# Optimization experiments

Hardware: AMD Instinct MI355X
Metric: run time of the kernel (lower is better)

Reference implementation:

```python
import jax, jax.numpy as jnp
import numpy as np

H = 16  # num_heads


def _sinusoidal_positions(n_pos, d, dtype=jnp.float32):
    half = d // 2
    freqs = 1.0 / 10000 ** (jnp.arange(0, half, dtype=dtype) / float(half))
    pos = jnp.arange(n_pos, dtype=dtype)[:, None]
    angles = pos * freqs[None, :]
    emb = jnp.concatenate([jnp.sin(angles), jnp.cos(angles)], axis=-1)
    if d % 2 == 1:
        emb = jnp.pad(emb, ((0, 0), (0, 1)))
    return emb.astype(dtype)


def setup_inputs() -> dict:
    key = jax.random.key(0)
    B, M, C = 64, 2048, 1024
    D = C // H
    ks = jax.random.split(key, 12)
    s = 1.0 / np.sqrt(C)
    return {
        "x": jax.random.normal(ks[0], (B, C), jnp.float32),
        "mem": jax.random.normal(ks[1], (B, M, C), jnp.float32),
        "Wq": jax.random.normal(ks[2], (C, C), jnp.float32) * s,
        "bq": jnp.zeros((C,), jnp.float32),
        "Wk": jax.random.normal(ks[3], (C, C), jnp.float32) * s,
        "bk": jnp.zeros((C,), jnp.float32),
        "Wv": jax.random.normal(ks[4], (C, C), jnp.float32) * s,
        "bv": jnp.zeros((C,), jnp.float32),
        "u_bias": jax.random.normal(ks[5], (H, D), jnp.float32) * 0.02,
        "v_bias": jax.random.normal(ks[6], (H, D), jnp.float32) * 0.02,
        "Wo": jax.random.normal(ks[7], (C, C), jnp.float32) * s,
        "bo": jnp.zeros((C,), jnp.float32),
    }


def reference(x, mem, Wq, bq, Wk, bk, Wv, bv, u_bias, v_bias, Wo, bo):
    B, C = x.shape
    D = C // H
    M = mem.shape[1]
    L = M + 1
    cat = jnp.concatenate([mem, x[:, None, :]], axis=1)  # (B, L, C)
    q = (x @ Wq + bq).reshape(B, H, D)
    k = (cat @ Wk + bk).reshape(B, L, H, D)
    v = (cat @ Wv + bv).reshape(B, L, H, D)
    r = _sinusoidal_positions(L, D)[::-1, :]  # (L, D), reversed
    scale = 1.0 / jnp.sqrt(jnp.float32(D))
    ac = jnp.einsum('bhd,blhd->bhl', q + u_bias[None, :, :], k)
    bd = jnp.einsum('bhd,ld->bhl', q + v_bias[None, :, :], r)
    attn = jax.nn.softmax((ac + bd) * scale, axis=-1)
    out = jnp.einsum('bhl,blhd->bhd', attn, v).reshape(B, C)
    return out @ Wo + bo
```

## Files before the change

kernel.cpp:

```cpp
#include <hip/hip_runtime.h>
#include <hip/hip_bf16.h>
#include <math.h>

#define B   64
#define C   1024
#define HH  16
#define DD  64
#define MM  2048
#define LL  2049
#define SCALE 0.125f
#define NCHC 9
#define CHC  228

template <int CTRL>
__device__ __forceinline__ float dpp_add(float keep, float send) {
  int moved =
      __builtin_amdgcn_update_dpp(0, __float_as_int(send), CTRL, 0xF, 0xF, true);
  return keep + __int_as_float(moved);
}

__global__ __launch_bounds__(256) void k_gemm(
    const float* __restrict__ A, int a_row_stride, int a_bx_off,
    const float* __restrict__ W, float* __restrict__ P) {
  __shared__ __attribute__((aligned(16))) float a_s[64 * 132];
  __shared__ __attribute__((aligned(16))) float b_s[128 * 68];
  int t = threadIdx.x;
  int jt = blockIdx.x, kc = blockIdx.y;
  const float* Ab = A + (size_t)jt * a_bx_off;
  int k0 = kc * 128;
  for (int idx = t; idx < 2048; idx += 256) {
    int bb = idx >> 5, f4 = idx & 31;
    float4 v = *(const float4*)&Ab[(size_t)bb * a_row_stride + k0 + 4 * f4];
    *(float4*)&a_s[bb * 132 + 4 * f4] = v;
  }
  for (int idx = t; idx < 2048; idx += 256) {
    int kk = idx >> 4, f4 = idx & 15;
    float4 v = *(const float4*)&W[(size_t)(k0 + kk) * 1024 + jt * 64 + 4 * f4];
    *(float4*)&b_s[kk * 68 + 4 * f4] = v;
  }
  __syncthreads();
  int j0 = (t & 15) * 4, b0 = (t >> 4) * 4;
  float4 acc[4];
#pragma unroll
  for (int i = 0; i < 4; ++i) acc[i] = make_float4(0.f, 0.f, 0.f, 0.f);
  for (int k = 0; k < 128; k += 4) {
    float4 w0 = *(const float4*)&b_s[(k + 0) * 68 + j0];
    float4 w1 = *(const float4*)&b_s[(k + 1) * 68 + j0];
    float4 w2 = *(const float4*)&b_s[(k + 2) * 68 + j0];
    float4 w3 = *(const float4*)&b_s[(k + 3) * 68 + j0];
#pragma unroll
    for (int i = 0; i < 4; ++i) {
      float4 av = *(const float4*)&a_s[(b0 + i) * 132 + k];
      acc[i].x += av.x * w0.x + av.y * w1.x + av.z * w2.x + av.w * w3.x;
      acc[i].y += av.x * w0.y + av.y * w1.y + av.z * w2.y + av.w * w3.y;
      acc[i].z += av.x * w0.z + av.y * w1.z + av.z * w2.z + av.w * w3.z;
      acc[i].w += av.x * w0.w + av.y * w1.w + av.z * w2.w + av.w * w3.w;
    }
  }
  size_t ob = (size_t)kc * 65536 + jt * 64;
#pragma unroll
  for (int i = 0; i < 4; ++i)
    *(float4*)&P[ob + (size_t)(b0 + i) * 1024 + j0] = acc[i];
}

__global__ __launch_bounds__(256) void k_reduce_qp(
    const float* __restrict__ P, const float* __restrict__ bq,
    const float* __restrict__ u, const float* __restrict__ v,
    float* __restrict__ qu, float* __restrict__ qv) {
  int idx = blockIdx.x * 256 + threadIdx.x;
  int b = idx >> 8, f4 = idx & 255;
  size_t off = (size_t)b * 1024 + 4 * f4;
  float4 s = *(const float4*)&P[off];
#pragma unroll
  for (int kc = 1; kc < 8; ++kc) {
    float4 t4 = *(const float4*)&P[(size_t)kc * 65536 + off];
    s.x += t4.x; s.y += t4.y; s.z += t4.z; s.w += t4.w;
  }
  float4 bb = *(const float4*)&bq[4 * f4];
  s.x += bb.x; s.y += bb.y; s.z += bb.z; s.w += bb.w;
  float4 uu = *(const float4*)&u[4 * f4];
  float4 vv = *(const float4*)&v[4 * f4];
  float4 o1 = make_float4(s.x + uu.x, s.y + uu.y, s.z + uu.z, s.w + uu.w);
  float4 o2 = make_float4(s.x + vv.x, s.y + vv.y, s.z + vv.z, s.w + vv.w);
  *(float4*)&qu[off] = o1;
  *(float4*)&qv[off] = o2;
}

__global__ __launch_bounds__(256) void k_reduce1(
    const float* __restrict__ P, const float* __restrict__ bias,
    float* __restrict__ out) {
  int idx = blockIdx.x * 256 + threadIdx.x;
  int b = idx >> 8, f4 = idx & 255;
  size_t off = (size_t)b * 1024 + 4 * f4;
  float4 s = *(const float4*)&P[off];
#pragma unroll
  for (int kc = 1; kc < 8; ++kc) {
    float4 t4 = *(const float4*)&P[(size_t)kc * 65536 + off];
    s.x += t4.x; s.y += t4.y; s.z += t4.z; s.w += t4.w;
  }
  float4 bb = *(const float4*)&bias[4 * f4];
  s.x += bb.x; s.y += bb.y; s.z += bb.z; s.w += bb.w;
  *(float4*)&out[off] = s;
}

__global__ __launch_bounds__(256) void k_wtilde(
    const float* __restrict__ qu, const float* __restrict__ Wk,
    float* __restrict__ wt) {
  __shared__ __attribute__((aligned(16))) float a_s[64 * 68];
  __shared__ __attribute__((aligned(16))) float w_s[64 * 68];
  int t = threadIdx.x, ct = blockIdx.x, h = blockIdx.y;
  for (int idx = t; idx < 1024; idx += 256) {
    int bb = idx >> 4, f4 = idx & 15;
    *(float4*)&a_s[bb * 68 + 4 * f4] =
        *(const float4*)&qu[(size_t)bb * 1024 + h * 64 + 4 * f4];
  }
  for (int idx = t; idx < 1024; idx += 256) {
    int cc = idx >> 4, f4 = idx & 15;
    *(float4*)&w_s[cc * 68 + 4 * f4] =
        *(const float4*)&Wk[(size_t)(ct * 64 + cc) * 1024 + h * 64 + 4 * f4];
  }
  __syncthreads();
  int c0 = (t & 15) * 4, b0 = (t >> 4) * 4;
  float acc[4][4] = {};
  for (int d = 0; d < 64; d += 4) {
    float4 w0 = *(const float4*)&w_s[(c0 + 0) * 68 + d];
    float4 w1 = *(const float4*)&w_s[(c0 + 1) * 68 + d];
    float4 w2 = *(const float4*)&w_s[(c0 + 2) * 68 + d];
    float4 w3 = *(const float4*)&w_s[(c0 + 3) * 68 + d];
#pragma unroll
    for (int i = 0; i < 4; ++i) {
      float4 av = *(const float4*)&a_s[(b0 + i) * 68 + d];
      acc[i][0] += av.x * w0.x + av.y * w0.y + av.z * w0.z + av.w * w0.w;
      acc[i][1] += av.x * w1.x + av.y * w1.y + av.z * w1.z + av.w * w1.w;
      acc[i][2] += av.x * w2.x + av.y * w2.y + av.z * w2.z + av.w * w2.w;
      acc[i][3] += av.x * w3.x + av.y * w3.y + av.z * w3.z + av.w * w3.w;
    }
  }
#pragma unroll
  for (int i = 0; i < 4; ++i) {
    float4 o = make_float4(acc[i][0], acc[i][1], acc[i][2], acc[i][3]);
    *(float4*)&wt[(size_t)((b0 + i) * 16 + h) * 1024 + ct * 64 + c0] = o;
  }
}

__global__ void k_rtab(float* __restrict__ rtab) {
  int idx = blockIdx.x * 256 + threadIdx.x;
  if (idx >= LL * 64) return;
  int l = idx >> 6, d = idx & 63;
  float p = (float)(LL - 1 - l);
  int dd = d & 31;
  float f = 1.0f / powf(10000.0f, (float)dd * (1.0f / 32.0f));
  float a = p * f;
  rtab[idx] = (d < 32) ? sinf(a) : cosf(a);
}

__global__ __launch_bounds__(256) void k_bd(
    const float* __restrict__ qv, const float* __restrict__ rtab,
    float* __restrict__ bd) {
  __shared__ __attribute__((aligned(16))) float rt_s[128 * 68];
  int t = threadIdx.x, ch = blockIdx.x, b = blockIdx.y;
  int l0 = ch * 128;
  int nrows = min(128, LL - l0);
  for (int idx = t; idx < nrows * 16; idx += 256) {
    int r = idx >> 4, d4 = idx & 15;
    *(float4*)&rt_s[r * 68 + 4 * d4] =
        *(const float4*)&rtab[(size_t)(l0 + r) * 64 + 4 * d4];
  }
  __syncthreads();
  for (int idx = t; idx < 16 * 128; idx += 256) {
    int h = idx >> 7, r = idx & 127;
    if (r < nrows) {
      const float* qh = &qv[(size_t)b * 1024 + h * 64];
      const float* rr = &rt_s[r * 68];
      float s = 0.f;
#pragma unroll
      for (int d4 = 0; d4 < 16; ++d4) {
        float4 rv = *(const float4*)&rr[4 * d4];
        float4 qq = *(const float4*)&qh[4 * d4];
        s += rv.x * qq.x + rv.y * qq.y + rv.z * qq.z + rv.w * qq.w;
      }
      bd[(size_t)(b * 16 + h) * LL + l0 + r] = s;
    }
  }
}

__global__ __launch_bounds__(256) void k_logits(
    const float* __restrict__ x, const float* __restrict__ mem,
    const float* __restrict__ wt, const float* __restrict__ bd,
    float* __restrict__ logits) {
  __shared__ float red_s[8 * 68];
  int t = threadIdx.x;
  int lane = t & 63, w = t >> 6;
  int b = blockIdx.y, ch = blockIdx.x;
  int l0 = ch * 128, lend = min(LL, l0 + 128);
  int c_off = w * 256 + lane * 4;
  float4 wr[16];
#pragma unroll
  for (int h = 0; h < 16; ++h)
    wr[h] = *(const float4*)&wt[(size_t)(b * 16 + h) * 1024 + c_off];
  const float* xrow = &x[(size_t)b * 1024 + c_off];
  const float* memb = &mem[(size_t)b * MM * 1024 + c_off];
  bool u0 = (lane & 1) != 0, u1 = (lane & 2) != 0;
  bool u2 = (lane & 4) != 0, u3 = (lane & 8) != 0;
  int hmap = ((lane & 1) << 3) | ((lane & 2) << 1) | ((lane & 4) >> 1) |
             ((lane & 8) >> 3);

  for (int g0 = l0; g0 < lend; g0 += 8) {
    int nr = min(8, lend - g0);
    float4 rb[8];
#pragma unroll
    for (int r = 0; r < 8; ++r) {
      int l = g0 + r;
      rb[r] = *(const float4*)((l < MM) ? &memb[(size_t)l * 1024] : xrow);
    }
#pragma unroll
    for (int r = 0; r < 8; ++r) {
      if (r < nr) {
        float4 rv = rb[r];
        float p[16];
#pragma unroll
        for (int h = 0; h < 16; ++h)
          p[h] = rv.x * wr[h].x + rv.y * wr[h].y + rv.z * wr[h].z +
                 rv.w * wr[h].w;
#pragma unroll
        for (int i = 0; i < 8; ++i) {
          float send = u0 ? p[i] : p[i + 8];
          float keep = u0 ? p[i + 8] : p[i];
          p[i] = dpp_add<0xB1>(keep, send);
        }
#pragma unroll
        for (int i = 0; i < 4; ++i) {
          float send = u1 ? p[i] : p[i + 4];
          float keep = u1 ? p[i + 4] : p[i];
          p[i] = dpp_add<0x4E>(keep, send);
        }
#pragma unroll
        for (int i = 0; i < 2; ++i) {
          float send = u2 ? p[i] : p[i + 2];
          float keep = u2 ? p[i + 2] : p[i];
          p[i] = keep + __shfl_xor(send, 4, 64);
        }
        {
          float send = u3 ? p[0] : p[1];
          float keep = u3 ? p[1] : p[0];
          float u = keep + __shfl_xor(send, 8, 64);
          u += __shfl_xor(u, 16, 64);
          u += __shfl_xor(u, 32, 64);
          if (lane < 16) red_s[r * 68 + w * 16 + hmap] = u;
        }
      }
    }
    __syncthreads();
    if (t < 128) {
      int r8 = t & 7, h = t >> 3;
      if (r8 < nr) {
        float s = red_s[r8 * 68 + h] + red_s[r8 * 68 + 16 + h] +
                  red_s[r8 * 68 + 32 + h] + red_s[r8 * 68 + 48 + h];
        int l = g0 + r8;
        size_t o = (size_t)(b * 16 + h) * LL + l;
        logits[o] = (s + bd[o]) * SCALE;
      }
    }
    __syncthreads();
  }
}

__global__ __launch_bounds__(256) void k_softmax(float* __restrict__ logits) {
  __shared__ float red[8];
  int t = threadIdx.x;
  size_t base = (size_t)blockIdx.x * LL;
  float rv[9];
  float m = -1e30f;
#pragma unroll
  for (int k = 0; k < 9; ++k) {
    int i = t + k * 256;
    rv[k] = (i < LL) ? logits[base + i] : -1e30f;
    m = fmaxf(m, rv[k]);
  }
#pragma unroll
  for (int s = 1; s < 64; s <<= 1) m = fmaxf(m, __shfl_xor(m, s, 64));
  if ((t & 63) == 0) red[t >> 6] = m;
  __syncthreads();
  m = fmaxf(fmaxf(red[0], red[1]), fmaxf(red[2], red[3]));
  float sum = 0.f;
#pragma unroll
  for (int k = 0; k < 9; ++k) {
    int i = t + k * 256;
    float e = __expf(rv[k] - m);
    rv[k] = e;
    if (i < LL) sum += e;
  }
#pragma unroll
  for (int s = 1; s < 64; s <<= 1) sum += __shfl_xor(sum, s, 64);
  if ((t & 63) == 0) red[4 + (t >> 6)] = sum;
  __syncthreads();
  float inv = 1.0f / (red[4] + red[5] + red[6] + red[7]);
#pragma unroll
  for (int k = 0; k < 9; ++k) {
    int i = t + k * 256;
    if (i < LL) logits[base + i] = rv[k] * inv;
  }
}

__global__ __launch_bounds__(256) void k_ctx(
    const float* __restrict__ x, const float* __restrict__ mem,
    const float* __restrict__ attn, float* __restrict__ part) {
  __shared__ __attribute__((aligned(16))) float att_s[CHC * 20];
  int t = threadIdx.x;
  int lane = t & 63, w = t >> 6;
  int b = blockIdx.y;
  int ch = blockIdx.x >> 2, cq = blockIdx.x & 3;
  int l0 = ch * CHC, lend = min(LL, l0 + CHC);
  int natt = lend - l0;
  int c_off = cq * 256 + lane * 4;
#pragma unroll
  for (int h = 0; h < 16; ++h)
    for (int r = t; r < natt; r += 256)
      att_s[r * 20 + h] = attn[(size_t)(b * 16 + h) * LL + l0 + r];
  __syncthreads();
  float4 acc[16];
#pragma unroll
  for (int i = 0; i < 16; ++i) acc[i] = make_float4(0.f, 0.f, 0.f, 0.f);
  const float* xrow = &x[(size_t)b * 1024 + c_off];
  const float* memb = &mem[(size_t)b * MM * 1024 + c_off];

  for (int g0 = l0 + w * 8; g0 < lend; g0 += 32) {
    int nr = min(8, lend - g0);
    float4 rb[8];
#pragma unroll
    for (int r = 0; r < 8; ++r) {
      int l = g0 + r;
      rb[r] = *(const float4*)((l < MM) ? &memb[(size_t)l * 1024] : xrow);
    }
#pragma unroll
    for (int r = 0; r < 8; ++r) {
      if (r < nr) {
        int ri = g0 + r - l0;
        const float4* a4 = (const float4*)&att_s[ri * 20];
        float4 aA = a4[0], aB = a4[1], aC = a4[2], aD = a4[3];
        float4 rv = rb[r];
#define ACC1(i, s)                                                       \
  acc[i].x += (s) * rv.x; acc[i].y += (s) * rv.y;                        \
  acc[i].z += (s) * rv.z; acc[i].w += (s) * rv.w;
        ACC1(0, aA.x) ACC1(1, aA.y) ACC1(2, aA.z) ACC1(3, aA.w)
        ACC1(4, aB.x) ACC1(5, aB.y) ACC1(6, aB.z) ACC1(7, aB.w)
        ACC1(8, aC.x) ACC1(9, aC.y) ACC1(10, aC.z) ACC1(11, aC.w)
        ACC1(12, aD.x) ACC1(13, aD.y) ACC1(14, aD.z) ACC1(15, aD.w)
#undef ACC1
      }
    }
  }
  __syncthreads();
  float* accb = att_s;
  for (int ww = 0; ww < 4; ++ww) {
    if (w == ww) {
      if (ww == 0) {
#pragma unroll
        for (int h = 0; h < 16; ++h)
          *(float4*)&accb[h * 256 + lane * 4] = acc[h];
      } else {
#pragma unroll
        for (int h = 0; h < 16; ++h) {
          float4 vv = *(const float4*)&accb[h * 256 + lane * 4];
          vv.x += acc[h].x; vv.y += acc[h].y;
          vv.z += acc[h].z; vv.w += acc[h].w;
          *(float4*)&accb[h * 256 + lane * 4] = vv;
        }
      }
    }
    __syncthreads();
  }
  size_t pb = (size_t)((b * NCHC + ch) * 16) * 1024 + cq * 256;
  for (int idx = t; idx < 1024; idx += 256) {
    int h = idx >> 6, c4 = idx & 63;
    *(float4*)&part[pb + (size_t)h * 1024 + 4 * c4] =
        *(const float4*)&accb[h * 256 + 4 * c4];
  }
}

__global__ __launch_bounds__(256) void k_ctxreduce(
    const float* __restrict__ part, float* __restrict__ ctx) {
  int o4 = blockIdx.x * 256 + threadIdx.x;
  size_t o = (size_t)o4 * 4;
  int b = (int)(o >> 14);
  int rem = (int)(o & 16383);
  const float* p = &part[(size_t)b * (NCHC * 16384) + rem];
  float4 s = *(const float4*)p;
#pragma unroll
  for (int chk = 1; chk < NCHC; ++chk) {
    float4 v = *(const float4*)&p[(size_t)chk * 16384];
    s.x += v.x; s.y += v.y; s.z += v.z; s.w += v.w;
  }
  *(float4*)&ctx[o] = s;
}

extern "C" void kernel_launch(void* const* d_in, const int* in_sizes, int n_in,
                              void* d_out, int out_size, void* d_ws,
                              size_t ws_size, hipStream_t stream) {
  const float* x = (const float*)d_in[0];
  const float* mem = (const float*)d_in[1];
  const float* Wq = (const float*)d_in[2];
  const float* bq = (const float*)d_in[3];
  const float* Wk = (const float*)d_in[4];
  const float* Wv = (const float*)d_in[6];
  const float* bv = (const float*)d_in[7];
  const float* u_bias = (const float*)d_in[8];
  const float* v_bias = (const float*)d_in[9];
  const float* Wo = (const float*)d_in[10];
  const float* bo = (const float*)d_in[11];
  float* out = (float*)d_out;

  float* ws = (float*)d_ws;
  float* qu = ws;
  float* qv = qu + 65536;
  float* logits = qv + 65536;
  float* ctx = logits + 2098176;
  float* out1 = ctx + 1048576;
  float* Bb = out1 + 65536;
  float* wt = Bb;
  float* rtab = Bb + 1048576;
  float* bd = Bb + 1179776;
  float* P = Bb + 3277952;
  float* part = Bb;

  k_gemm<<<dim3(16, 8), 256, 0, stream>>>(x, 1024, 0, Wq, P);
  k_rtab<<<dim3(513), 256, 0, stream>>>(rtab);
  k_reduce_qp<<<dim3(64), 256, 0, stream>>>(P, bq, u_bias, v_bias, qu, qv);
  k_wtilde<<<dim3(16, 16), 256, 0, stream>>>(qu, Wk, wt);
  k_bd<<<dim3(17, 64), 256, 0, stream>>>(qv, rtab, bd);
  k_logits<<<dim3(17, 64), 256, 0, stream>>>(x, mem, wt, bd, logits);
  k_softmax<<<dim3(1024), 256, 0, stream>>>(logits);
  k_ctx<<<dim3(36, 64), 256, 0, stream>>>(x, mem, logits, part);
  k_ctxreduce<<<dim3(1024), 256, 0, stream>>>(part, ctx);
  k_gemm<<<dim3(16, 8), 256, 0, stream>>>(ctx, 16384, 1024, Wv, P);
  k_reduce1<<<dim3(64), 256, 0, stream>>>(P, bv, out1);
  k_gemm<<<dim3(16, 8), 256, 0, stream>>>(out1, 1024, 0, Wo, P);
  k_reduce1<<<dim3(64), 256, 0, stream>>>(P, bo, out);
}
```

Measured before the change: 401.8 us.

## Fuse logits, softmax and context into one flash-style pass over mem

Merges the logits, softmax and context kernels into one online-softmax kernel that reads each mem row once. The row feeds both the score dot products and the weighted accumulation, where before mem was streamed twice. Per-chunk max and sum are written out, and a new combine kernel rescales and sums the 17 chunk partials into ctx. The bd table is stored in a position-major layout to suit the fused kernel. In exchange, each 8-row group adds extra barriers and accumulator rescaling, and register pressure under launch_bounds(256,2) may limit occupancy.

Result: slower. 453.5 us (+12.9%).

```diff
diff --git a/kernel.cpp b/kernel.cpp
--- a/kernel.cpp
+++ b/kernel.cpp
@@ -9,8 +9,7 @@
 #define MM  2048
 #define LL  2049
 #define SCALE 0.125f
-#define NCHC 9
-#define CHC  228
+#define NCH 17
 
 template <int CTRL>
 __device__ __forceinline__ float dpp_add(float keep, float send) {
@@ -156,7 +155,7 @@
 
 __global__ __launch_bounds__(256) void k_bd(
     const float* __restrict__ qv, const float* __restrict__ rtab,
-    float* __restrict__ bd) {
+    float* __restrict__ bdt) {
   __shared__ __attribute__((aligned(16))) float rt_s[128 * 68];
   int t = threadIdx.x, ch = blockIdx.x, b = blockIdx.y;
   int l0 = ch * 128;
@@ -168,7 +167,7 @@
   }
   __syncthreads();
   for (int idx = t; idx < 16 * 128; idx += 256) {
-    int h = idx >> 7, r = idx & 127;
+    int r = idx >> 4, h = idx & 15;
     if (r < nrows) {
       const float* qh = &qv[(size_t)b * 1024 + h * 64];
       const float* rr = &rt_s[r * 68];
@@ -179,16 +178,19 @@
         float4 qq = *(const float4*)&qh[4 * d4];
         s += rv.x * qq.x + rv.y * qq.y + rv.z * qq.z + rv.w * qq.w;
       }
-      bd[(size_t)(b * 16 + h) * LL + l0 + r] = s;
-    }
-  }
-}
-
-__global__ __launch_bounds__(256) void k_logits(
+      bdt[((size_t)b * LL + l0 + r) * 16 + h] = s;
+    }
+  }
+}
+
+__global__ __launch_bounds__(256, 2) void k_fattn(
     const float* __restrict__ x, const float* __restrict__ mem,
-    const float* __restrict__ wt, const float* __restrict__ bd,
-    float* __restrict__ logits) {
+    const float* __restrict__ wt, const float* __restrict__ bdt,
+    float* __restrict__ part, float* __restrict__ ms) {
   __shared__ float red_s[8 * 68];
+  __shared__ __attribute__((aligned(16))) float p_s[8 * 20];
+  __shared__ __attribute__((aligned(16))) float f_s[16];
+  __shared__ float ms_s[32];
   int t = threadIdx.x;
   int lane = t & 63, w = t >> 6;
   int b = blockIdx.y, ch = blockIdx.x;
@@ -204,13 +206,21 @@
   bool u2 = (lane & 4) != 0, u3 = (lane & 8) != 0;
   int hmap = ((lane & 1) << 3) | ((lane & 2) << 1) | ((lane & 4) >> 1) |
              ((lane & 8) >> 3);
+  float4 acc[16];
+#pragma unroll
+  for (int i = 0; i < 16; ++i) acc[i] = make_float4(0.f, 0.f, 0.f, 0.f);
+  if (t < 16) {
+    ms_s[t * 2] = -3e38f;
+    ms_s[t * 2 + 1] = 0.f;
+  }
+  __syncthreads();
 
   for (int g0 = l0; g0 < lend; g0 += 8) {
     int nr = min(8, lend - g0);
     float4 rb[8];
 #pragma unroll
     for (int r = 0; r < 8; ++r) {
-      int l = g0 + r;
+      int l = min(g0 + r, LL - 1);
       rb[r] = *(const float4*)((l < MM) ? &memb[(size_t)l * 1024] : xrow);
     }
 #pragma unroll
@@ -253,145 +263,103 @@
     __syncthreads();
     if (t < 128) {
       int r8 = t & 7, h = t >> 3;
+      float lo = -3e38f;
       if (r8 < nr) {
         float s = red_s[r8 * 68 + h] + red_s[r8 * 68 + 16 + h] +
                   red_s[r8 * 68 + 32 + h] + red_s[r8 * 68 + 48 + h];
-        int l = g0 + r8;
-        size_t o = (size_t)(b * 16 + h) * LL + l;
-        logits[o] = (s + bd[o]) * SCALE;
+        lo = (s + bdt[((size_t)b * LL + g0 + r8) * 16 + h]) * SCALE;
       }
+      float tm = lo;
+      tm = fmaxf(tm, __shfl_xor(tm, 1, 64));
+      tm = fmaxf(tm, __shfl_xor(tm, 2, 64));
+      tm = fmaxf(tm, __shfl_xor(tm, 4, 64));
+      float m_old = ms_s[h * 2];
+      float m_new = fmaxf(m_old, tm);
+      float pe = __expf(lo - m_new);
+      p_s[r8 * 20 + h] = pe;
+      float srow = pe;
+      srow += __shfl_xor(srow, 1, 64);
+      srow += __shfl_xor(srow, 2, 64);
+      srow += __shfl_xor(srow, 4, 64);
+      if (r8 == 0) {
+        float f = __expf(m_old - m_new);
+        ms_s[h * 2] = m_new;
+        ms_s[h * 2 + 1] = ms_s[h * 2 + 1] * f + srow;
+        f_s[h] = f;
+      }
     }
     __syncthreads();
-  }
-}
-
-__global__ __launch_bounds__(256) void k_softmax(float* __restrict__ logits) {
-  __shared__ float red[8];
-  int t = threadIdx.x;
-  size_t base = (size_t)blockIdx.x * LL;
-  float rv[9];
-  float m = -1e30f;
-#pragma unroll
-  for (int k = 0; k < 9; ++k) {
-    int i = t + k * 256;
-    rv[k] = (i < LL) ? logits[base + i] : -1e30f;
-    m = fmaxf(m, rv[k]);
-  }
-#pragma unroll
-  for (int s = 1; s < 64; s <<= 1) m = fmaxf(m, __shfl_xor(m, s, 64));
-  if ((t & 63) == 0) red[t >> 6] = m;
-  __syncthreads();
-  m = fmaxf(fmaxf(red[0], red[1]), fmaxf(red[2], red[3]));
-  float sum = 0.f;
-#pragma unroll
-  for (int k = 0; k < 9; ++k) {
-    int i = t + k * 256;
-    float e = __expf(rv[k] - m);
-    rv[k] = e;
-    if (i < LL) sum += e;
-  }
-#pragma unroll
-  for (int s = 1; s < 64; s <<= 1) sum += __shfl_xor(sum, s, 64);
-  if ((t & 63) == 0) red[4 + (t >> 6)] = sum;
-  __syncthreads();
-  float inv = 1.0f / (red[4] + red[5] + red[6] + red[7]);
-#pragma unroll
-  for (int k = 0; k < 9; ++k) {
-    int i = t + k * 256;
-    if (i < LL) logits[base + i] = rv[k] * inv;
-  }
-}
-
-__global__ __launch_bounds__(256) void k_ctx(
-    const float* __restrict__ x, const float* __restrict__ mem,
-    const float* __restrict__ attn, float* __restrict__ part) {
-  __shared__ __attribute__((aligned(16))) float att_s[CHC * 20];
-  int t = threadIdx.x;
-  int lane = t & 63, w = t >> 6;
-  int b = blockIdx.y;
-  int ch = blockIdx.x >> 2, cq = blockIdx.x & 3;
-  int l0 = ch * CHC, lend = min(LL, l0 + CHC);
-  int natt = lend - l0;
-  int c_off = cq * 256 + lane * 4;
-#pragma unroll
-  for (int h = 0; h < 16; ++h)
-    for (int r = t; r < natt; r += 256)
-      att_s[r * 20 + h] = attn[(size_t)(b * 16 + h) * LL + l0 + r];
-  __syncthreads();
-  float4 acc[16];
-#pragma unroll
-  for (int i = 0; i < 16; ++i) acc[i] = make_float4(0.f, 0.f, 0.f, 0.f);
-  const float* xrow = &x[(size_t)b * 1024 + c_off];
-  const float* memb = &mem[(size_t)b * MM * 1024 + c_off];
-
-  for (int g0 = l0 + w * 8; g0 < lend; g0 += 32) {
-    int nr = min(8, lend - g0);
-    float4 rb[8];
-#pragma unroll
-    for (int r = 0; r < 8; ++r) {
-      int l = g0 + r;
-      rb[r] = *(const float4*)((l < MM) ? &memb[(size_t)l * 1024] : xrow);
+    {
+      float4 f0 = *(const float4*)&f_s[0];
+      float4 f1 = *(const float4*)&f_s[4];
+      float4 f2 = *(const float4*)&f_s[8];
+      float4 f3 = *(const float4*)&f_s[12];
+#define RS(i, fv)                                                        \
+  acc[i].x *= (fv); acc[i].y *= (fv); acc[i].z *= (fv); acc[i].w *= (fv);
+      RS(0, f0.x) RS(1, f0.y) RS(2, f0.z) RS(3, f0.w)
+      RS(4, f1.x) RS(5, f1.y) RS(6, f1.z) RS(7, f1.w)
+      RS(8, f2.x) RS(9, f2.y) RS(10, f2.z) RS(11, f2.w)
+      RS(12, f3.x) RS(13, f3.y) RS(14, f3.z) RS(15, f3.w)
+#undef RS
     }
 #pragma unroll
     for (int r = 0; r < 8; ++r) {
       if (r < nr) {
-        int ri = g0 + r - l0;
-        const float4* a4 = (const float4*)&att_s[ri * 20];
-        float4 aA = a4[0], aB = a4[1], aC = a4[2], aD = a4[3];
+        const float4* pp = (const float4*)&p_s[r * 20];
+        float4 pA = pp[0], pB = pp[1], pC = pp[2], pD = pp[3];
         float4 rv = rb[r];
 #define ACC1(i, s)                                                       \
   acc[i].x += (s) * rv.x; acc[i].y += (s) * rv.y;                        \
   acc[i].z += (s) * rv.z; acc[i].w += (s) * rv.w;
-        ACC1(0, aA.x) ACC1(1, aA.y) ACC1(2, aA.z) ACC1(3, aA.w)
-        ACC1(4, aB.x) ACC1(5, aB.y) ACC1(6, aB.z) ACC1(7, aB.w)
-        ACC1(8, aC.x) ACC1(9, aC.y) ACC1(10, aC.z) ACC1(11, aC.w)
-        ACC1(12, aD.x) ACC1(13, aD.y) ACC1(14, aD.z) ACC1(15, aD.w)
+        ACC1(0, pA.x) ACC1(1, pA.y) ACC1(2, pA.z) ACC1(3, pA.w)
+        ACC1(4, pB.x) ACC1(5, pB.y) ACC1(6, pB.z) ACC1(7, pB.w)
+        ACC1(8, pC.x) ACC1(9, pC.y) ACC1(10, pC.z) ACC1(11, pC.w)
+        ACC1(12, pD.x) ACC1(13, pD.y) ACC1(14, pD.z) ACC1(15, pD.w)
 #undef ACC1
       }
     }
   }
-  __syncthreads();
-  float* accb = att_s;
-  for (int ww = 0; ww < 4; ++ww) {
-    if (w == ww) {
-      if (ww == 0) {
-#pragma unroll
-        for (int h = 0; h < 16; ++h)
-          *(float4*)&accb[h * 256 + lane * 4] = acc[h];
-      } else {
-#pragma unroll
-        for (int h = 0; h < 16; ++h) {
-          float4 vv = *(const float4*)&accb[h * 256 + lane * 4];
-          vv.x += acc[h].x; vv.y += acc[h].y;
-          vv.z += acc[h].z; vv.w += acc[h].w;
-          *(float4*)&accb[h * 256 + lane * 4] = vv;
-        }
-      }
-    }
-    __syncthreads();
-  }
-  size_t pb = (size_t)((b * NCHC + ch) * 16) * 1024 + cq * 256;
-  for (int idx = t; idx < 1024; idx += 256) {
-    int h = idx >> 6, c4 = idx & 63;
-    *(float4*)&part[pb + (size_t)h * 1024 + 4 * c4] =
-        *(const float4*)&accb[h * 256 + 4 * c4];
-  }
-}
-
-__global__ __launch_bounds__(256) void k_ctxreduce(
-    const float* __restrict__ part, float* __restrict__ ctx) {
-  int o4 = blockIdx.x * 256 + threadIdx.x;
-  size_t o = (size_t)o4 * 4;
-  int b = (int)(o >> 14);
-  int rem = (int)(o & 16383);
-  const float* p = &part[(size_t)b * (NCHC * 16384) + rem];
-  float4 s = *(const float4*)p;
-#pragma unroll
-  for (int chk = 1; chk < NCHC; ++chk) {
-    float4 v = *(const float4*)&p[(size_t)chk * 16384];
-    s.x += v.x; s.y += v.y; s.z += v.z; s.w += v.w;
-  }
-  *(float4*)&ctx[o] = s;
+  size_t pb = ((size_t)(b * NCH + ch) * 16) * 1024;
+#pragma unroll
+  for (int h = 0; h < 16; ++h)
+    *(float4*)&part[pb + (size_t)h * 1024 + c_off] = acc[h];
+  if (t < 16) {
+    ms[((size_t)(b * NCH + ch) * 16 + t) * 2 + 0] = ms_s[t * 2];
+    ms[((size_t)(b * NCH + ch) * 16 + t) * 2 + 1] = ms_s[t * 2 + 1];
+  }
+}
+
+__global__ __launch_bounds__(256) void k_combine(
+    const float* __restrict__ part, const float* __restrict__ ms,
+    float* __restrict__ ctx) {
+  __shared__ float ms_l[NCH * 32];
+  __shared__ float wsc[NCH * 16];
+  int t = threadIdx.x, cq = blockIdx.x, b = blockIdx.y;
+  for (int i = t; i < NCH * 32; i += 256) ms_l[i] = ms[(size_t)b * NCH * 32 + i];
+  __syncthreads();
+  if (t < 16) {
+    float M = -3e38f;
+#pragma unroll
+    for (int ch = 0; ch < NCH; ++ch) M = fmaxf(M, ms_l[ch * 32 + t * 2]);
+    float den = 0.f;
+#pragma unroll
+    for (int ch = 0; ch < NCH; ++ch)
+      den += __expf(ms_l[ch * 32 + t * 2] - M) * ms_l[ch * 32 + t * 2 + 1];
+    float inv = 1.0f / den;
+#pragma unroll
+    for (int ch = 0; ch < NCH; ++ch)
+      wsc[ch * 16 + t] = __expf(ms_l[ch * 32 + t * 2] - M) * inv;
+  }
+  __syncthreads();
+  int c = cq * 256 + t;
+  for (int h = 0; h < 16; ++h) {
+    float acc = 0.f;
+#pragma unroll
+    for (int ch = 0; ch < NCH; ++ch)
+      acc += wsc[ch * 16 + h] *
+             part[((size_t)(b * NCH + ch) * 16 + h) * 1024 + c];
+    ctx[(size_t)(b * 16 + h) * 1024 + c] = acc;
+  }
 }
 
 extern "C" void kernel_launch(void* const* d_in, const int* in_sizes, int n_in,
@@ -413,25 +381,22 @@
   float* ws = (float*)d_ws;
   float* qu = ws;
   float* qv = qu + 65536;
-  float* logits = qv + 65536;
-  float* ctx = logits + 2098176;
+  float* wt = qv + 65536;
+  float* rtab = wt + 1048576;
+  float* bdt = rtab + 131200;
+  float* P = bdt + 2098176;
+  float* ctx = P + 524288;
   float* out1 = ctx + 1048576;
-  float* Bb = out1 + 65536;
-  float* wt = Bb;
-  float* rtab = Bb + 1048576;
-  float* bd = Bb + 1179776;
-  float* P = Bb + 3277952;
-  float* part = Bb;
+  float* ms = out1 + 65536;
+  float* part = ms + 34816;
 
   k_gemm<<<dim3(16, 8), 256, 0, stream>>>(x, 1024, 0, Wq, P);
   k_rtab<<<dim3(513), 256, 0, stream>>>(rtab);
   k_reduce_qp<<<dim3(64), 256, 0, stream>>>(P, bq, u_bias, v_bias, qu, qv);
   k_wtilde<<<dim3(16, 16), 256, 0, stream>>>(qu, Wk, wt);
-  k_bd<<<dim3(17, 64), 256, 0, stream>>>(qv, rtab, bd);
-  k_logits<<<dim3(17, 64), 256, 0, stream>>>(x, mem, wt, bd, logits);
-  k_softmax<<<dim3(1024), 256, 0, stream>>>(logits);
-  k_ctx<<<dim3(36, 64), 256, 0, stream>>>(x, mem, logits, part);
-  k_ctxreduce<<<dim3(1024), 256, 0, stream>>>(part, ctx);
+  k_bd<<<dim3(17, 64), 256, 0, stream>>>(qv, rtab, bdt);
+  k_fattn<<<dim3(NCH, 64), 256, 0, stream>>>(x, mem, wt, bdt, part, ms);
+  k_combine<<<dim3(4, 64), 256, 0, stream>>>(part, ms, ctx);
   k_gemm<<<dim3(16, 8), 256, 0, stream>>>(ctx, 16384, 1024, Wv, P);
   k_reduce1<<<dim3(64), 256, 0, stream>>>(P, bv, out1);
   k_gemm<<<dim3(16, 8), 256, 0, stream>>>(out1, 1024, 0, Wo, P);
```

## Fuse softmax into logits and ctx via online per-chunk max/sum statistics

Applied to the files above, without the earlier changes.

Removes the separate softmax kernel. The logits kernel now records a running max and exp-sum per head for each chunk, and the ctx kernel combines those statistics to normalise the logits on the fly. Logits and bd are stored in an [l][h] layout so the ctx kernel's shared-memory fill reads contiguous memory. This saves one launch and a full read-write pass over the logits, at the cost of extra exp and shuffle work inside the logits loop and a redundant statistics combine in every ctx block.

Result: slower. 440.7 us (+9.7%).

```diff
diff --git a/kernel.cpp b/kernel.cpp
--- a/kernel.cpp
+++ b/kernel.cpp
@@ -9,6 +9,8 @@
 #define MM  2048
 #define LL  2049
 #define SCALE 0.125f
+#define NCH 17
+#define LROWS 2176
 #define NCHC 9
 #define CHC  228
 
@@ -156,7 +158,7 @@
 
 __global__ __launch_bounds__(256) void k_bd(
     const float* __restrict__ qv, const float* __restrict__ rtab,
-    float* __restrict__ bd) {
+    float* __restrict__ bdt) {
   __shared__ __attribute__((aligned(16))) float rt_s[128 * 68];
   int t = threadIdx.x, ch = blockIdx.x, b = blockIdx.y;
   int l0 = ch * 128;
@@ -168,7 +170,7 @@
   }
   __syncthreads();
   for (int idx = t; idx < 16 * 128; idx += 256) {
-    int h = idx >> 7, r = idx & 127;
+    int r = idx >> 4, h = idx & 15;
     if (r < nrows) {
       const float* qh = &qv[(size_t)b * 1024 + h * 64];
       const float* rr = &rt_s[r * 68];
@@ -179,16 +181,17 @@
         float4 qq = *(const float4*)&qh[4 * d4];
         s += rv.x * qq.x + rv.y * qq.y + rv.z * qq.z + rv.w * qq.w;
       }
-      bd[(size_t)(b * 16 + h) * LL + l0 + r] = s;
+      bdt[((size_t)b * LL + l0 + r) * 16 + h] = s;
     }
   }
 }
 
 __global__ __launch_bounds__(256) void k_logits(
     const float* __restrict__ x, const float* __restrict__ mem,
-    const float* __restrict__ wt, const float* __restrict__ bd,
-    float* __restrict__ logits) {
+    const float* __restrict__ wt, const float* __restrict__ bdt,
+    float* __restrict__ logits_t, float* __restrict__ ms) {
   __shared__ float red_s[8 * 68];
+  __shared__ float ms_s[32];
   int t = threadIdx.x;
   int lane = t & 63, w = t >> 6;
   int b = blockIdx.y, ch = blockIdx.x;
@@ -204,6 +207,11 @@
   bool u2 = (lane & 4) != 0, u3 = (lane & 8) != 0;
   int hmap = ((lane & 1) << 3) | ((lane & 2) << 1) | ((lane & 4) >> 1) |
              ((lane & 8) >> 3);
+  if (t < 16) {
+    ms_s[t * 2] = -3e38f;
+    ms_s[t * 2 + 1] = 0.f;
+  }
+  __syncthreads();
 
   for (int g0 = l0; g0 < lend; g0 += 8) {
     int nr = min(8, lend - g0);
@@ -253,59 +261,45 @@
     __syncthreads();
     if (t < 128) {
       int r8 = t & 7, h = t >> 3;
+      float lo = -3e38f;
       if (r8 < nr) {
         float s = red_s[r8 * 68 + h] + red_s[r8 * 68 + 16 + h] +
                   red_s[r8 * 68 + 32 + h] + red_s[r8 * 68 + 48 + h];
         int l = g0 + r8;
-        size_t o = (size_t)(b * 16 + h) * LL + l;
-        logits[o] = (s + bd[o]) * SCALE;
+        lo = (s + bdt[((size_t)b * LL + l) * 16 + h]) * SCALE;
+        logits_t[((size_t)b * LROWS + l) * 16 + h] = lo;
+      }
+      float tm = lo;
+      tm = fmaxf(tm, __shfl_xor(tm, 1, 64));
+      tm = fmaxf(tm, __shfl_xor(tm, 2, 64));
+      tm = fmaxf(tm, __shfl_xor(tm, 4, 64));
+      float m_old = ms_s[h * 2];
+      float m_new = fmaxf(m_old, tm);
+      float pe = (r8 < nr) ? __expf(lo - m_new) : 0.f;
+      float srow = pe;
+      srow += __shfl_xor(srow, 1, 64);
+      srow += __shfl_xor(srow, 2, 64);
+      srow += __shfl_xor(srow, 4, 64);
+      if (r8 == 0) {
+        float f = __expf(m_old - m_new);
+        ms_s[h * 2] = m_new;
+        ms_s[h * 2 + 1] = ms_s[h * 2 + 1] * f + srow;
       }
     }
     __syncthreads();
   }
-}
-
-__global__ __launch_bounds__(256) void k_softmax(float* __restrict__ logits) {
-  __shared__ float red[8];
-  int t = threadIdx.x;
-  size_t base = (size_t)blockIdx.x * LL;
-  float rv[9];
-  float m = -1e30f;
-#pragma unroll
-  for (int k = 0; k < 9; ++k) {
-    int i = t + k * 256;
-    rv[k] = (i < LL) ? logits[base + i] : -1e30f;
-    m = fmaxf(m, rv[k]);
-  }
-#pragma unroll
-  for (int s = 1; s < 64; s <<= 1) m = fmaxf(m, __shfl_xor(m, s, 64));
-  if ((t & 63) == 0) red[t >> 6] = m;
-  __syncthreads();
-  m = fmaxf(fmaxf(red[0], red[1]), fmaxf(red[2], red[3]));
-  float sum = 0.f;
-#pragma unroll
-  for (int k = 0; k < 9; ++k) {
-    int i = t + k * 256;
-    float e = __expf(rv[k] - m);
-    rv[k] = e;
-    if (i < LL) sum += e;
-  }
-#pragma unroll
-  for (int s = 1; s < 64; s <<= 1) sum += __shfl_xor(sum, s, 64);
-  if ((t & 63) == 0) red[4 + (t >> 6)] = sum;
-  __syncthreads();
-  float inv = 1.0f / (red[4] + red[5] + red[6] + red[7]);
-#pragma unroll
-  for (int k = 0; k < 9; ++k) {
-    int i = t + k * 256;
-    if (i < LL) logits[base + i] = rv[k] * inv;
+  if (t < 16) {
+    ms[((size_t)(b * NCH + ch) * 16 + t) * 2 + 0] = ms_s[t * 2];
+    ms[((size_t)(b * NCH + ch) * 16 + t) * 2 + 1] = ms_s[t * 2 + 1];
   }
 }
 
 __global__ __launch_bounds__(256) void k_ctx(
     const float* __restrict__ x, const float* __restrict__ mem,
-    const float* __restrict__ attn, float* __restrict__ part) {
+    const float* __restrict__ logits_t, const float* __restrict__ ms,
+    float* __restrict__ part) {
   __shared__ __attribute__((aligned(16))) float att_s[CHC * 20];
+  __shared__ float m_l[16], inv_l[16];
   int t = threadIdx.x;
   int lane = t & 63, w = t >> 6;
   int b = blockIdx.y;
@@ -313,10 +307,25 @@
   int l0 = ch * CHC, lend = min(LL, l0 + CHC);
   int natt = lend - l0;
   int c_off = cq * 256 + lane * 4;
-#pragma unroll
-  for (int h = 0; h < 16; ++h)
-    for (int r = t; r < natt; r += 256)
-      att_s[r * 20 + h] = attn[(size_t)(b * 16 + h) * LL + l0 + r];
+  if (t < 16) {
+    float M = -3e38f;
+#pragma unroll
+    for (int cc = 0; cc < NCH; ++cc)
+      M = fmaxf(M, ms[((size_t)(b * NCH + cc) * 16 + t) * 2]);
+    float den = 0.f;
+#pragma unroll
+    for (int cc = 0; cc < NCH; ++cc)
+      den += __expf(ms[((size_t)(b * NCH + cc) * 16 + t) * 2] - M) *
+             ms[((size_t)(b * NCH + cc) * 16 + t) * 2 + 1];
+    m_l[t] = M;
+    inv_l[t] = 1.0f / den;
+  }
+  __syncthreads();
+  for (int idx = t; idx < natt * 16; idx += 256) {
+    int r = idx >> 4, h = idx & 15;
+    float lo = logits_t[((size_t)b * LROWS + l0 + r) * 16 + h];
+    att_s[r * 20 + h] = __expf(lo - m_l[h]) * inv_l[h];
+  }
   __syncthreads();
   float4 acc[16];
 #pragma unroll
@@ -413,24 +422,23 @@
   float* ws = (float*)d_ws;
   float* qu = ws;
   float* qv = qu + 65536;
-  float* logits = qv + 65536;
-  float* ctx = logits + 2098176;
+  float* wt = qv + 65536;
+  float* rtab = wt + 1048576;
+  float* bdt = rtab + 131200;
+  float* logits_t = bdt + 2098176;
+  float* ms = logits_t + 2228224;
+  float* P = ms + 34816;
+  float* ctx = P + 524288;
   float* out1 = ctx + 1048576;
-  float* Bb = out1 + 65536;
-  float* wt = Bb;
-  float* rtab = Bb + 1048576;
-  float* bd = Bb + 1179776;
-  float* P = Bb + 3277952;
-  float* part = Bb;
+  float* part = out1 + 65536;
 
   k_gemm<<<dim3(16, 8), 256, 0, stream>>>(x, 1024, 0, Wq, P);
   k_rtab<<<dim3(513), 256, 0, stream>>>(rtab);
   k_reduce_qp<<<dim3(64), 256, 0, stream>>>(P, bq, u_bias, v_bias, qu, qv);
   k_wtilde<<<dim3(16, 16), 256, 0, stream>>>(qu, Wk, wt);
-  k_bd<<<dim3(17, 64), 256, 0, stream>>>(qv, rtab, bd);
-  k_logits<<<dim3(17, 64), 256, 0, stream>>>(x, mem, wt, bd, logits);
-  k_softmax<<<dim3(1024), 256, 0, stream>>>(logits);
-  k_ctx<<<dim3(36, 64), 256, 0, stream>>>(x, mem, logits, part);
+  k_bd<<<dim3(17, 64), 256, 0, stream>>>(qv, rtab, bdt);
+  k_logits<<<dim3(NCH, 64), 256, 0, stream>>>(x, mem, wt, bdt, logits_t, ms);
+  k_ctx<<<dim3(36, 64), 256, 0, stream>>>(x, mem, logits_t, ms, part);
   k_ctxreduce<<<dim3(1024), 256, 0, stream>>>(part, ctx);
   k_gemm<<<dim3(16, 8), 256, 0, stream>>>(ctx, 16384, 1024, Wv, P);
   k_reduce1<<<dim3(64), 256, 0, stream>>>(P, bv, out1);
```
